# Performance work log

Measured on AMD Instinct MI355X. Metric: run time of the kernel, lower is better.

The kernel has to match this reference:

```python
import jax, jax.numpy as jnp
import numpy as np

S = 1024          # tokens (prefill)
DIM = 2560
HEAD_DIM = 128
N_HEADS = 20
N_KV = 5
HPG = N_HEADS // N_KV      # heads per kv group = 4
GS = 128                   # weight-scale group size
THETA = 500000.0
EPS = 1e-05
QKV_OUT = (N_HEADS + 2 * N_KV) * HEAD_DIM  # 3840


def setup_inputs() -> dict:
    key = jax.random.key(0)
    ks = jax.random.split(key, 7)
    x = jax.random.normal(ks[0], (S, DIM), jnp.float32)
    # unpacked int2 (ternary) weights, stored as float for the reference math
    w_qkv = jax.random.randint(ks[1], (QKV_OUT, DIM), -1, 2).astype(jnp.float32)
    ws_qkv = jax.random.uniform(ks[2], (QKV_OUT, DIM // GS), jnp.float32, 0.01, 0.05)
    w_o = jax.random.randint(ks[3], (DIM, N_HEADS * HEAD_DIM), -1, 2).astype(jnp.float32)
    ws_o = jax.random.uniform(ks[4], (DIM, N_HEADS * HEAD_DIM // GS), jnp.float32, 0.01, 0.05)
    q_norm_w = 1.0 + 0.02 * jax.random.normal(ks[5], (HEAD_DIM,), jnp.float32)
    k_norm_w = 1.0 + 0.02 * jax.random.normal(ks[6], (HEAD_DIM,), jnp.float32)
    return {"x": x, "w_qkv": w_qkv, "ws_qkv": ws_qkv, "w_o": w_o, "ws_o": ws_o,
            "q_norm_w": q_norm_w, "k_norm_w": k_norm_w}


def _quant_act(x):
    # per-token symmetric int8 quant: s = 127 / max|x| (clamped)
    s = 127.0 / jnp.clip(jnp.max(jnp.abs(x), axis=-1, keepdims=True), 1e-05, None)
    q = jnp.clip(jnp.round(x * s), -128.0, 127.0)
    return q, s


def _bitlinear(x, w, ws):
    # int8 activation x int2 weight GEMM with per-(out,group) dequant scales
    q, s = _quant_act(x)
    w_dq = w * jnp.repeat(ws, GS, axis=1)        # [out, in]
    return (q @ w_dq.T) / s


def _rmsnorm(x, w):
    return x * jax.lax.rsqrt(jnp.mean(x * x, axis=-1, keepdims=True) + EPS) * w


def _rope(x, cos, sin):
    # x: [S, ..., d]; cos/sin: [S, d//2], interleaved-pair (llama) convention
    d2 = x.shape[-1] // 2
    shape = (x.shape[0],) + (1,) * (x.ndim - 2) + (d2,)
    c = cos.reshape(shape)
    s = sin.reshape(shape)
    xr = x.reshape(x.shape[:-1] + (d2, 2))
    x0, x1 = xr[..., 0], xr[..., 1]
    out = jnp.stack([x0 * c - x1 * s, x0 * s + x1 * c], axis=-1)
    return out.reshape(x.shape)


def reference(x, w_qkv, ws_qkv, w_o, ws_o, q_norm_w, k_norm_w):
    qkv = _bitlinear(x, w_qkv, ws_qkv)                       # [S, 3840]
    q_size = N_HEADS * HEAD_DIM
    k_size = N_KV * HEAD_DIM
    xq = qkv[:, :q_size].reshape(S, N_KV, HPG, HEAD_DIM)     # [S, g, h, d]
    xk = qkv[:, q_size:q_size + k_size].reshape(S, N_KV, HEAD_DIM)
    xv = qkv[:, q_size + k_size:].reshape(S, N_KV, HEAD_DIM)
    xq = _rmsnorm(xq, q_norm_w)
    xk = _rmsnorm(xk, k_norm_w)
    # RoPE (prefill: positions 0..S-1)
    pos = jnp.arange(S, dtype=jnp.float32)
    inv_freq = THETA ** (-jnp.arange(0, HEAD_DIM, 2, dtype=jnp.float32) / HEAD_DIM)
    ang = pos[:, None] * inv_freq[None, :]                   # [S, d/2]
    cos, sin = jnp.cos(ang), jnp.sin(ang)
    xq = _rope(xq, cos, sin)
    xk = _rope(xk, cos, sin)
    # GQA causal flash-attention math
    scale = HEAD_DIM ** -0.5
    scores = jnp.einsum('sghd,tgd->ghst', xq, xk) * scale    # [g, h, S, S]
    causal = jnp.tril(jnp.ones((S, S), bool))
    scores = jnp.where(causal, scores, -1e30)
    attn = jax.nn.softmax(scores, axis=-1)
    out = jnp.einsum('ghst,tgd->sghd', attn, xv).reshape(S, N_HEADS * HEAD_DIM)
    return _bitlinear(out, w_o, ws_o)                        # [S, DIM]
```

## Files before the change

kernel.cpp:

```cpp
#include <hip/hip_runtime.h>
#include <hip/hip_bf16.h>
#include <cstdint>
#include <math.h>

#define SEQ 1024
#define DIM 2560
#define HD 128
#define NH 20
#define NKV 5
#define QKV_OUT 3840
#define GS 128

typedef __bf16 bf16;
typedef __bf16 bf16x4 __attribute__((ext_vector_type(4)));
typedef __bf16 bf16x8 __attribute__((ext_vector_type(8)));
typedef float f32x4 __attribute__((ext_vector_type(4)));

__global__ __launch_bounds__(256) void fused_pre(
    const float* __restrict__ x, bf16* __restrict__ act, float* __restrict__ rs,
    const float* __restrict__ w1, const float* __restrict__ ws1, bf16* __restrict__ o1,
    float* __restrict__ rope, long n1_4) {
  const int tid = threadIdx.x;
  if (blockIdx.x < SEQ) {
    const int row = blockIdx.x;
    const float* xr = x + (size_t)row * DIM;
    float m = 0.f;
    for (int i = tid; i < DIM; i += 256) m = fmaxf(m, fabsf(xr[i]));
    for (int off = 32; off; off >>= 1) m = fmaxf(m, __shfl_xor(m, off));
    __shared__ float red[4];
    __shared__ float s_bc;
    if ((tid & 63) == 0) red[tid >> 6] = m;
    __syncthreads();
    if (tid == 0) {
      float mm = fmaxf(fmaxf(red[0], red[1]), fmaxf(red[2], red[3]));
      mm = fmaxf(mm, 1e-5f);
      s_bc = 127.f / mm;
      rs[row] = mm / 127.f;
    }
    __syncthreads();
    const float s = s_bc;
    bf16* ar = act + (size_t)row * DIM;
    for (int i = tid; i < DIM; i += 256) {
      float q = rintf(xr[i] * s);
      q = fminf(fmaxf(q, -128.f), 127.f);
      ar[i] = (bf16)q;
    }
  } else {
    long i = (long)(blockIdx.x - SEQ) * 256 + tid;
    if (i < n1_4) {
      long e = i * 4;
      int row = (int)(e / DIM);
      int k = (int)(e % DIM);
      float sc = ws1[(size_t)row * (DIM / GS) + (k / GS)];
      float4 wv = *(const float4*)(w1 + e);
      bf16x4 ov;
      ov[0] = (bf16)(wv.x * sc);
      ov[1] = (bf16)(wv.y * sc);
      ov[2] = (bf16)(wv.z * sc);
      ov[3] = (bf16)(wv.w * sc);
      *(bf16x4*)(o1 + e) = ov;
    } else {
      long u = i - n1_4;
      if (u >= (long)SEQ * 64) return;
      int t = (int)(u >> 6), fi = (int)(u & 63);
      float inv_freq = powf(500000.f, -(float)(2 * fi) * (1.f / 128.f));
      float ang = (float)t * inv_freq;
      float sn, cs;
      sincosf(ang, &sn, &cs);
      rope[u * 2] = cs;
      rope[u * 2 + 1] = sn;
    }
  }
}

__device__ __forceinline__ void gload_lds16(const bf16* g, bf16* l) {
  __builtin_amdgcn_global_load_lds(
      (const __attribute__((address_space(1))) void*)g,
      (__attribute__((address_space(3))) void*)l, 16, 0, 0);
}

template <int BM, int BN>
__global__ __launch_bounds__(256) void gemm_pipe(
    const bf16* __restrict__ A, const bf16* __restrict__ B,
    const float* __restrict__ rs, float* __restrict__ C,
    int N, int K, int Kh, size_t part_stride, int ND, int NN) {
  constexpr int MI = BM / 32;
  constexpr int NW = BN / 32;
  constexpr int APASS = BM / 32;
  constexpr int BPASS = BN / 32;
  __shared__ bf16 As[2][BM * 64];
  __shared__ bf16 Bs[2][BN * 64];
  const int b = (int)blockIdx.x;
  const int mtile = b / ND;
  const int nz = b % ND;
  const int ntile = nz % NN;
  const int z = nz / NN;
  const int tid = threadIdx.x;
  const int w = tid >> 6, l = tid & 63;
  const int row0 = mtile * BM;
  const int col0 = ntile * BN;
  const int wm = (w >> 1) * (BM / 2), wn = (w & 1) * (BN / 2);
  const int lcol = l & 15, quad = l >> 4;
  const int sr = l >> 3, sg = l & 7;
  const bf16* Ag = A + (size_t)row0 * K + (size_t)z * Kh;
  const bf16* Bg = B + (size_t)col0 * K + (size_t)z * Kh;

  f32x4 acc[MI][NW] = {};

#define STAGE_AB(buf, k0)                                                      \
  {                                                                            \
    _Pragma("unroll") for (int i = 0; i < APASS; ++i) {                        \
      int rb = w * (BM / 4) + i * 8;                                           \
      int r = rb + sr;                                                         \
      gload_lds16(Ag + (size_t)r * K + (k0) + ((sg ^ (r & 7)) * 8),            \
                  &As[buf][rb * 64]);                                          \
    }                                                                          \
    _Pragma("unroll") for (int i = 0; i < BPASS; ++i) {                        \
      int rb = w * (BN / 4) + i * 8;                                           \
      int r = rb + sr;                                                         \
      gload_lds16(Bg + (size_t)r * K + (k0) + ((sg ^ (r & 7)) * 8),            \
                  &Bs[buf][rb * 64]);                                          \
    }                                                                          \
  }

  STAGE_AB(0, 0)
  __syncthreads();

  int buf = 0;
  for (int k0 = 0; k0 < Kh; k0 += 64) {
    if (k0 + 64 < Kh) STAGE_AB(buf ^ 1, k0 + 64)
#pragma unroll
    for (int ks = 0; ks < 2; ++ks) {
      bf16x8 af[MI], bff[NW];
#pragma unroll
      for (int mi = 0; mi < MI; ++mi) {
        int R = wm + mi * 16 + lcol;
        af[mi] = *(const bf16x8*)(&As[buf][R * 64 + (((ks * 4 + quad) ^ (R & 7)) * 8)]);
      }
#pragma unroll
      for (int ni = 0; ni < NW; ++ni) {
        int R = wn + ni * 16 + lcol;
        bff[ni] = *(const bf16x8*)(&Bs[buf][R * 64 + (((ks * 4 + quad) ^ (R & 7)) * 8)]);
      }
#pragma unroll
      for (int mi = 0; mi < MI; ++mi)
#pragma unroll
        for (int ni = 0; ni < NW; ++ni)
          acc[mi][ni] = __builtin_amdgcn_mfma_f32_16x16x32_bf16(
              af[mi], bff[ni], acc[mi][ni], 0, 0, 0);
    }
    __syncthreads();
    buf ^= 1;
  }
#undef STAGE_AB

  float* Cp = C + (size_t)z * part_stride;
#pragma unroll
  for (int mi = 0; mi < MI; ++mi) {
#pragma unroll
    for (int ni = 0; ni < NW; ++ni) {
      int col = col0 + wn + ni * 16 + lcol;
#pragma unroll
      for (int r = 0; r < 4; ++r) {
        int row = row0 + wm + mi * 16 + quad * 4 + r;
        Cp[(size_t)row * N + col] = acc[mi][ni][r] * rs[row];
      }
    }
  }
}

__global__ __launch_bounds__(256) void fused_post(
    const float* __restrict__ qkvA, const float* __restrict__ qkvB,
    const float* __restrict__ qw, const float* __restrict__ kw,
    const float* __restrict__ rope,
    bf16* __restrict__ Qo, bf16* __restrict__ Ko, bf16* __restrict__ Vt) {
  __shared__ bf16 Ls[64 * 137];
  const int bx = (int)blockIdx.x;
  const int tid = threadIdx.x;
  if (bx < 6400) {
    const int wave = tid >> 6, i = tid & 63;
    const int u = bx * 4 + wave;
    const int t = u & 1023, h = u >> 10;
    const size_t off = (h < NH)
        ? (size_t)t * QKV_OUT + h * HD
        : (size_t)t * QKV_OUT + 2560 + (h - NH) * HD;
    const float* s1 = qkvA + off;
    const float* s2 = qkvB + off;
    float2 xa = *(const float2*)(s1 + 2 * i);
    float2 xb = *(const float2*)(s2 + 2 * i);
    float x0 = xa.x + xb.x;
    float x1 = xa.y + xb.y;
    float ss = x0 * x0 + x1 * x1;
    for (int off2 = 1; off2 < 64; off2 <<= 1) ss += __shfl_xor(ss, off2);
    float r = rsqrtf(ss * (1.f / 128.f) + 1e-5f);
    const float* wv = (h < NH) ? qw : kw;
    float y0 = x0 * r * wv[2 * i];
    float y1 = x1 * r * wv[2 * i + 1];
    float2 csn = *(const float2*)(rope + ((size_t)t * 64 + i) * 2);
    float cs = csn.x, sn = csn.y;
    float o0 = y0 * cs - y1 * sn;
    float o1 = y0 * sn + y1 * cs;
    if (h < NH) {
      bf16* dst = Qo + ((size_t)t * NH + h) * HD + 2 * i;
      dst[0] = (bf16)o0; dst[1] = (bf16)o1;
    } else {
      bf16* dst = Ko + ((size_t)(h - NH) * SEQ + t) * HD + 2 * i;
      dst[0] = (bf16)o0; dst[1] = (bf16)o1;
    }
  } else {
    const int b2 = bx - 6400;
    const int t0 = (b2 & 15) * 64, g = b2 >> 4;
    {
      const int tl = tid >> 4;
      const int d0 = (tid & 15) * 8;
#pragma unroll
      for (int pass = 0; pass < 4; ++pass) {
        int t = pass * 16 + tl;
        size_t off = (size_t)(t0 + t) * QKV_OUT + 3200 + g * HD + d0;
        float4 a = *(const float4*)(qkvA + off);
        float4 b = *(const float4*)(qkvA + off + 4);
        float4 a2 = *(const float4*)(qkvB + off);
        float4 b2v = *(const float4*)(qkvB + off + 4);
        bf16* dst = Ls + t * 137 + d0;
        dst[0] = (bf16)(a.x + a2.x); dst[1] = (bf16)(a.y + a2.y);
        dst[2] = (bf16)(a.z + a2.z); dst[3] = (bf16)(a.w + a2.w);
        dst[4] = (bf16)(b.x + b2v.x); dst[5] = (bf16)(b.y + b2v.y);
        dst[6] = (bf16)(b.z + b2v.z); dst[7] = (bf16)(b.w + b2v.w);
      }
    }
    __syncthreads();
    {
      const int dl = tid >> 3;
      const int tl0 = (tid & 7) * 8;
#pragma unroll
      for (int pass = 0; pass < 4; ++pass) {
        int d = pass * 32 + dl;
        bf16x8 v;
#pragma unroll
        for (int j = 0; j < 8; ++j) v[j] = Ls[(tl0 + j) * 137 + d];
        *(bf16x8*)(Vt + ((size_t)g * HD + d) * SEQ + t0 + tl0) = v;
      }
    }
  }
}

__global__ __launch_bounds__(256, 1) void attn_mfma(
    const bf16* __restrict__ Qb, const bf16* __restrict__ Kb,
    const bf16* __restrict__ Vt, float* __restrict__ Op,
    float* __restrict__ ml,
    const float* __restrict__ w2, const float* __restrict__ ws2,
    bf16* __restrict__ o2) {
  const int bxi = (int)blockIdx.x;
  const int tid = threadIdx.x;
  if (bxi >= 600) {
    const long b2 = bxi - 600;
    const long base4 = b2 * 1024 + tid;
#pragma unroll
    for (int it = 0; it < 4; ++it) {
      long e = (base4 + it * 256) * 4;
      int row = (int)(e / DIM);
      int k = (int)(e % DIM);
      float sc = ws2[(size_t)row * (DIM / GS) + (k / GS)];
      float4 wv = *(const float4*)(w2 + e);
      bf16x4 ov;
      ov[0] = (bf16)(wv.x * sc);
      ov[1] = (bf16)(wv.y * sc);
      ov[2] = (bf16)(wv.z * sc);
      ov[3] = (bf16)(wv.w * sc);
      *(bf16x4*)(o2 + e) = ov;
    }
    return;
  }
  const int p = bxi % 60;
  const int hp = bxi / 60;
  int qb, c;
  if (p < 24)      { qb = 31 - p / 3;            c = p % 3; }
  else if (p < 48) { int r = p - 24; qb = 23 - (r >> 1); c = r & 1; }
  else             { qb = 59 - p;                c = 0; }
  const int wave = tid >> 6, lane = tid & 63;
  const int H = (hp >> 1) * 4 + (hp & 1) * 2 + (wave >> 1);
  const int g = H >> 2;
  const int qcol = lane & 15, quad = lane >> 4;
  const int q_tok = qb * 32 + (wave & 1) * 16 + qcol;
  const float scale = 0.08838834764831843f;

  __shared__ bf16 Ks[2][64 * 128];
  __shared__ bf16 Vs[2][128 * 64];

  const bf16* kbase = Kb + (size_t)g * SEQ * HD;
  const bf16* vbase = Vt + (size_t)g * HD * SEQ;

  bf16x8 qf[4];
  {
    const bf16* qp = Qb + ((size_t)q_tok * NH + H) * HD + quad * 8;
#pragma unroll
    for (int kc = 0; kc < 4; ++kc) qf[kc] = *(const bf16x8*)(qp + kc * 32);
  }

  float m_i = -1e30f, l_i = 0.f;
  f32x4 o_acc[8] = {};
  const int kt0 = c * 6;
  int kt_max = kt0 + 5;
  {
    int ktg = (qb * 32 + 31) >> 6;
    if (ktg < kt_max) kt_max = ktg;
  }

  const int k_r = lane >> 4, k_g = lane & 15;
  const int v_r = lane >> 3, v_g = lane & 7;

#define STAGE(buf, key0)                                                       \
  {                                                                            \
    _Pragma("unroll") for (int p2 = 0; p2 < 4; ++p2) {                         \
      int r0 = wave * 16 + p2 * 4;                                             \
      int r = r0 + k_r;                                                        \
      gload_lds16(kbase + (size_t)((key0) + r) * HD + ((k_g ^ (r & 15)) * 8),  \
                  &Ks[buf][r0 * 128]);                                         \
    }                                                                          \
    _Pragma("unroll") for (int p2 = 0; p2 < 4; ++p2) {                         \
      int r0 = wave * 32 + p2 * 8;                                             \
      int r = r0 + v_r;                                                        \
      gload_lds16(vbase + (size_t)r * SEQ + (key0) + ((v_g ^ (r & 7)) * 8),    \
                  &Vs[buf][r0 * 64]);                                          \
    }                                                                          \
  }

  STAGE(0, kt0 * 64)

  for (int kt = kt0; kt <= kt_max; ++kt) {
    const int key0 = kt * 64;
    __syncthreads();
    if (kt < kt_max) STAGE((kt + 1) & 1, key0 + 64)
    const bf16* Kt = Ks[kt & 1];
    const bf16* Vtile = Vs[kt & 1];

    bf16x8 kf[4][4];
#pragma unroll
    for (int mg = 0; mg < 4; ++mg) {
      const int R = mg * 16 + qcol;
      const bf16* krow = Kt + R * 128;
#pragma unroll
      for (int kc = 0; kc < 4; ++kc)
        kf[mg][kc] = *(const bf16x8*)(krow + (((kc * 4 + quad) ^ (R & 15)) * 8));
    }
    f32x4 s[4];
#pragma unroll
    for (int mg = 0; mg < 4; ++mg) {
      f32x4 acc = {0.f, 0.f, 0.f, 0.f};
#pragma unroll
      for (int kc = 0; kc < 4; ++kc)
        acc = __builtin_amdgcn_mfma_f32_16x16x32_bf16(kf[mg][kc], qf[kc], acc, 0, 0, 0);
      s[mg] = acc;
    }

    bf16x8 vf[8][2];
#pragma unroll
    for (int mg2 = 0; mg2 < 8; ++mg2) {
      const int R = mg2 * 16 + qcol;
      const bf16* vrow = Vtile + R * 64;
#pragma unroll
      for (int cc = 0; cc < 2; ++cc) {
        int g8a = cc * 8 + quad;
        int g8b = cc * 8 + 4 + quad;
        bf16x4 v0 = *(const bf16x4*)(vrow + ((g8a >> 1) ^ (R & 7)) * 8 + (g8a & 1) * 4);
        bf16x4 v1 = *(const bf16x4*)(vrow + ((g8b >> 1) ^ (R & 7)) * 8 + (g8b & 1) * 4);
#pragma unroll
        for (int j = 0; j < 4; ++j) { vf[mg2][cc][j] = v0[j]; vf[mg2][cc][j + 4] = v1[j]; }
      }
    }

    float mt = -1e30f;
#pragma unroll
    for (int mg = 0; mg < 4; ++mg)
#pragma unroll
      for (int r = 0; r < 4; ++r) {
        int key = key0 + mg * 16 + quad * 4 + r;
        float v = (key <= q_tok) ? s[mg][r] * scale : -1e30f;
        s[mg][r] = v;
        mt = fmaxf(mt, v);
      }
    mt = fmaxf(mt, __shfl_xor(mt, 16));
    mt = fmaxf(mt, __shfl_xor(mt, 32));
    float mnew = fmaxf(m_i, mt);
    float alpha = __expf(m_i - mnew);
    float ps = 0.f;
#pragma unroll
    for (int mg = 0; mg < 4; ++mg)
#pragma unroll
      for (int r = 0; r < 4; ++r) {
        float pv = __expf(s[mg][r] - mnew);
        s[mg][r] = pv;
        ps += pv;
      }
    ps += __shfl_xor(ps, 16);
    ps += __shfl_xor(ps, 32);
    l_i = l_i * alpha + ps;
    m_i = mnew;
#pragma unroll
    for (int mg2 = 0; mg2 < 8; ++mg2)
#pragma unroll
      for (int r = 0; r < 4; ++r) o_acc[mg2][r] *= alpha;

    bf16x8 pb[2];
#pragma unroll
    for (int cc = 0; cc < 2; ++cc)
#pragma unroll
      for (int j = 0; j < 8; ++j)
        pb[cc][j] = (bf16)s[cc * 2 + (j >> 2)][j & 3];

#pragma unroll
    for (int mg2 = 0; mg2 < 8; ++mg2) {
      f32x4 acc = o_acc[mg2];
#pragma unroll
      for (int cc = 0; cc < 2; ++cc)
        acc = __builtin_amdgcn_mfma_f32_16x16x32_bf16(vf[mg2][cc], pb[cc], acc, 0, 0, 0);
      o_acc[mg2] = acc;
    }
  }
#undef STAGE

  float* op = Op + ((size_t)c * SEQ + q_tok) * DIM + (size_t)H * HD + quad * 4;
#pragma unroll
  for (int mg2 = 0; mg2 < 8; ++mg2)
    *(f32x4*)(op + mg2 * 16) = o_acc[mg2];
  if (lane < 16) {
    size_t mloff = (((size_t)c * SEQ + q_tok) * NH + H) * 2;
    ml[mloff] = m_i;
    ml[mloff + 1] = l_i;
  }
}

__global__ __launch_bounds__(256) void merge_quant(
    const float* __restrict__ Op, const float* __restrict__ ml,
    bf16* __restrict__ act, float* __restrict__ rs) {
  const int t = blockIdx.x;
  const int tid = threadIdx.x;
  const int nc = (((t | 31) >> 6) / 6) + 1;
  __shared__ float sw[3][NH];
  __shared__ float red[4];
  __shared__ float s_bc;
  if (tid < NH) {
    const size_t base = ((size_t)t * NH + tid) * 2;
    const size_t cs = (size_t)SEQ * NH * 2;
    float m0 = ml[base], l0 = ml[base + 1];
    float m1 = 0.f, l1 = 0.f, m2 = 0.f, l2 = 0.f;
    float M = m0;
    if (nc > 1) { m1 = ml[base + cs];     l1 = ml[base + cs + 1];     M = fmaxf(M, m1); }
    if (nc > 2) { m2 = ml[base + 2 * cs]; l2 = ml[base + 2 * cs + 1]; M = fmaxf(M, m2); }
    float w0 = __expf(m0 - M), w1 = 0.f, w2 = 0.f;
    float L = w0 * l0;
    if (nc > 1) { w1 = __expf(m1 - M); L += w1 * l1; }
    if (nc > 2) { w2 = __expf(m2 - M); L += w2 * l2; }
    const float invL = 1.f / L;
    sw[0][tid] = w0 * invL;
    sw[1][tid] = w1 * invL;
    sw[2][tid] = w2 * invL;
  }
  __syncthreads();
  float vals[10];
  float amax = 0.f;
  const float* ob = Op + (size_t)t * DIM;
  const size_t cs = (size_t)SEQ * DIM;
#pragma unroll
  for (int j = 0; j < 10; ++j) {
    int d = j * 256 + tid;
    int h = d >> 7;
    float v = ob[d] * sw[0][h];
    if (nc > 1) v += ob[d + cs] * sw[1][h];
    if (nc > 2) v += ob[d + 2 * cs] * sw[2][h];
    vals[j] = v;
    amax = fmaxf(amax, fabsf(v));
  }
  for (int off = 32; off; off >>= 1) amax = fmaxf(amax, __shfl_xor(amax, off));
  if ((tid & 63) == 0) red[tid >> 6] = amax;
  __syncthreads();
  if (tid == 0) {
    float mm = fmaxf(fmaxf(red[0], red[1]), fmaxf(red[2], red[3]));
    mm = fmaxf(mm, 1e-5f);
    s_bc = 127.f / mm;
    rs[t] = mm / 127.f;
  }
  __syncthreads();
  const float s = s_bc;
  bf16* ar = act + (size_t)t * DIM;
#pragma unroll
  for (int j = 0; j < 10; ++j) {
    float q = rintf(vals[j] * s);
    q = fminf(fmaxf(q, -128.f), 127.f);
    ar[j * 256 + tid] = (bf16)q;
  }
}

extern "C" void kernel_launch(void* const* d_in, const int* in_sizes, int n_in,
                              void* d_out, int out_size, void* d_ws, size_t ws_size,
                              hipStream_t stream) {
  const float* x      = (const float*)d_in[0];
  const float* w_qkv  = (const float*)d_in[1];
  const float* ws_qkv = (const float*)d_in[2];
  const float* w_o    = (const float*)d_in[3];
  const float* ws_o   = (const float*)d_in[4];
  const float* qnw    = (const float*)d_in[5];
  const float* knw    = (const float*)d_in[6];
  float* out = (float*)d_out;

  char* p = (char*)d_ws;
  bf16*  act1 = (bf16*)p;  p += (size_t)SEQ * DIM * 2;
  float* rs1  = (float*)p; p += 4096;
  bf16*  wqdq = (bf16*)p;  p += (size_t)QKV_OUT * DIM * 2;
  bf16*  wodq = (bf16*)p;  p += (size_t)DIM * DIM * 2;
  float* qkvA = (float*)p; p += (size_t)SEQ * QKV_OUT * 4;
  float* qkvB = (float*)p; p += (size_t)SEQ * QKV_OUT * 4;
  bf16*  Qb   = (bf16*)p;  p += (size_t)SEQ * NH * HD * 2;
  bf16*  Kb   = (bf16*)p;  p += (size_t)NKV * SEQ * HD * 2;
  bf16*  Vt   = (bf16*)p;  p += (size_t)NKV * HD * SEQ * 2;
  bf16*  act2 = (bf16*)p;  p += (size_t)SEQ * DIM * 2;
  float* rs2  = (float*)p; p += 4096;
  float* rope = (float*)p; p += (size_t)SEQ * 64 * 2 * 4;
  float* Opart = (float*)p; p += (size_t)3 * SEQ * DIM * 4;
  float* mlbuf = (float*)p; p += (size_t)3 * SEQ * NH * 2 * 4;

  {
    long n1_4 = (long)QKV_OUT * DIM / 4;
    int dq_blocks = (int)((n1_4 + 255) / 256);
    int rope_blocks = (SEQ * 64 + 255) / 256;
    fused_pre<<<SEQ + dq_blocks + rope_blocks, 256, 0, stream>>>(
        x, act1, rs1, w_qkv, ws_qkv, wqdq, rope, n1_4);
  }
  gemm_pipe<128, 128><<<480, 256, 0, stream>>>(
      act1, wqdq, rs1, qkvA, QKV_OUT, DIM, DIM / 2, (size_t)SEQ * QKV_OUT, 60, 30);
  fused_post<<<6480, 256, 0, stream>>>(qkvA, qkvB, qnw, knw, rope, Qb, Kb, Vt);
  attn_mfma<<<2200, 256, 0, stream>>>(Qb, Kb, Vt, Opart, mlbuf, w_o, ws_o, wodq);
  merge_quant<<<SEQ, 256, 0, stream>>>(Opart, mlbuf, act2, rs2);
  gemm_pipe<64, 64><<<640, 256, 0, stream>>>(
      act2, wodq, rs2, out, DIM, DIM, DIM, 0, 40, 40);
}
```

Baseline: 217.7 us.

## Use split-K atomic GEMM with larger tiles for output projection

Replaces the 64x64 output-projection GEMM with a 128x128-tile kernel that splits K into four parts and accumulates partial results into the output with float atomics. The output buffer is zeroed by extra blocks appended to the attention launch. The aim is more data reuse per tile while keeping enough blocks to fill the GPU. The cost is atomic traffic, the extra zeroing work, and a summation order that is no longer deterministic.

```diff
diff --git a/kernel.cpp b/kernel.cpp
--- a/kernel.cpp
+++ b/kernel.cpp
@@ -164,6 +164,85 @@
       for (int r = 0; r < 4; ++r) {
         int row = row0 + wm + mi * 16 + quad * 4 + r;
         Cp[(size_t)row * N + col] = acc[mi][ni][r] * rs[row];
+      }
+    }
+  }
+}
+
+template <int BM, int BN>
+__global__ __launch_bounds__(256, 3) void gemm_atomic(
+    const bf16* __restrict__ A, const bf16* __restrict__ B,
+    const float* __restrict__ rs, float* __restrict__ C,
+    int N, int K, int Kh, int ND, int NN) {
+  constexpr int MI = BM / 32;
+  constexpr int NW = BN / 32;
+  constexpr int APASS = BM / 32;
+  constexpr int BPASS = BN / 32;
+  __shared__ bf16 As[BM * 64];
+  __shared__ bf16 Bs[BN * 64];
+  const int b = (int)blockIdx.x;
+  const int mtile = b / ND;
+  const int nz = b % ND;
+  const int ntile = nz % NN;
+  const int z = nz / NN;
+  const int tid = threadIdx.x;
+  const int w = tid >> 6, l = tid & 63;
+  const int row0 = mtile * BM;
+  const int col0 = ntile * BN;
+  const int wm = (w >> 1) * (BM / 2), wn = (w & 1) * (BN / 2);
+  const int lcol = l & 15, quad = l >> 4;
+  const int sr = l >> 3, sg = l & 7;
+  const bf16* Ag = A + (size_t)row0 * K + (size_t)z * Kh;
+  const bf16* Bg = B + (size_t)col0 * K + (size_t)z * Kh;
+
+  f32x4 acc[MI][NW] = {};
+
+  for (int k0 = 0; k0 < Kh; k0 += 64) {
+#pragma unroll
+    for (int i = 0; i < APASS; ++i) {
+      int rb = w * (BM / 4) + i * 8;
+      int r = rb + sr;
+      gload_lds16(Ag + (size_t)r * K + k0 + ((sg ^ (r & 7)) * 8), &As[rb * 64]);
+    }
+#pragma unroll
+    for (int i = 0; i < BPASS; ++i) {
+      int rb = w * (BN / 4) + i * 8;
+      int r = rb + sr;
+      gload_lds16(Bg + (size_t)r * K + k0 + ((sg ^ (r & 7)) * 8), &Bs[rb * 64]);
+    }
+    __syncthreads();
+#pragma unroll
+    for (int ks = 0; ks < 2; ++ks) {
+      bf16x8 af[MI], bff[NW];
+#pragma unroll
+      for (int mi = 0; mi < MI; ++mi) {
+        int R = wm + mi * 16 + lcol;
+        af[mi] = *(const bf16x8*)(&As[R * 64 + (((ks * 4 + quad) ^ (R & 7)) * 8)]);
+      }
+#pragma unroll
+      for (int ni = 0; ni < NW; ++ni) {
+        int R = wn + ni * 16 + lcol;
+        bff[ni] = *(const bf16x8*)(&Bs[R * 64 + (((ks * 4 + quad) ^ (R & 7)) * 8)]);
+      }
+#pragma unroll
+      for (int mi = 0; mi < MI; ++mi)
+#pragma unroll
+        for (int ni = 0; ni < NW; ++ni)
+          acc[mi][ni] = __builtin_amdgcn_mfma_f32_16x16x32_bf16(
+              af[mi], bff[ni], acc[mi][ni], 0, 0, 0);
+    }
+    __syncthreads();
+  }
+
+#pragma unroll
+  for (int mi = 0; mi < MI; ++mi) {
+#pragma unroll
+    for (int ni = 0; ni < NW; ++ni) {
+      int col = col0 + wn + ni * 16 + lcol;
+#pragma unroll
+      for (int r = 0; r < 4; ++r) {
+        int row = row0 + wm + mi * 16 + quad * 4 + r;
+        unsafeAtomicAdd(&C[(size_t)row * N + col], acc[mi][ni][r] * rs[row]);
       }
     }
   }
@@ -249,9 +328,17 @@
     const bf16* __restrict__ Vt, float* __restrict__ Op,
     float* __restrict__ ml,
     const float* __restrict__ w2, const float* __restrict__ ws2,
-    bf16* __restrict__ o2) {
+    bf16* __restrict__ o2, float* __restrict__ outz) {
   const int bxi = (int)blockIdx.x;
   const int tid = threadIdx.x;
+  if (bxi >= 2200) {
+    const long b2 = bxi - 2200;
+    f32x4 zv = {0.f, 0.f, 0.f, 0.f};
+    f32x4* dst = (f32x4*)outz + b2 * 1024 + tid;
+#pragma unroll
+    for (int it = 0; it < 4; ++it) dst[it * 256] = zv;
+    return;
+  }
   if (bxi >= 600) {
     const long b2 = bxi - 600;
     const long base4 = b2 * 1024 + tid;
@@ -529,8 +616,8 @@
   gemm_pipe<128, 128><<<480, 256, 0, stream>>>(
       act1, wqdq, rs1, qkvA, QKV_OUT, DIM, DIM / 2, (size_t)SEQ * QKV_OUT, 60, 30);
   fused_post<<<6480, 256, 0, stream>>>(qkvA, qkvB, qnw, knw, rope, Qb, Kb, Vt);
-  attn_mfma<<<2200, 256, 0, stream>>>(Qb, Kb, Vt, Opart, mlbuf, w_o, ws_o, wodq);
+  attn_mfma<<<2840, 256, 0, stream>>>(Qb, Kb, Vt, Opart, mlbuf, w_o, ws_o, wodq, out);
   merge_quant<<<SEQ, 256, 0, stream>>>(Opart, mlbuf, act2, rs2);
-  gemm_pipe<64, 64><<<640, 256, 0, stream>>>(
-      act2, wodq, rs2, out, DIM, DIM, DIM, 0, 40, 40);
-}
+  gemm_atomic<128, 128><<<640, 256, 0, stream>>>(
+      act2, wodq, rs2, out, DIM, DIM, DIM / 4, 80, 20);
+}
```

New measurement: 233.8 us. +7.4%, slower.

## Fuse QKV weight dequantization into the GEMM B-tile loads

Applied to the files above, without the earlier changes.

Removes the separate pass that dequantized the fp32 QKV weights to a bf16 workspace. The QKV GEMM now reads fp32 weights and group scales directly into registers, converts them to bf16, and writes them to LDS one stage ahead of use. This saves a full write and re-read of the dequantized weight matrix. In exchange, each of the 480 blocks (grid 8 row tiles by 60 column/K-split slots) converts fp32 weight tiles again, so every weight element is read as fp32 and converted 8 times. Register-staged loads also replace the async global-to-LDS path for B.

```diff
diff --git a/kernel.cpp b/kernel.cpp
--- a/kernel.cpp
+++ b/kernel.cpp
@@ -18,8 +18,7 @@
 
 __global__ __launch_bounds__(256) void fused_pre(
     const float* __restrict__ x, bf16* __restrict__ act, float* __restrict__ rs,
-    const float* __restrict__ w1, const float* __restrict__ ws1, bf16* __restrict__ o1,
-    float* __restrict__ rope, long n1_4) {
+    float* __restrict__ rope) {
   const int tid = threadIdx.x;
   if (blockIdx.x < SEQ) {
     const int row = blockIdx.x;
@@ -46,30 +45,15 @@
       ar[i] = (bf16)q;
     }
   } else {
-    long i = (long)(blockIdx.x - SEQ) * 256 + tid;
-    if (i < n1_4) {
-      long e = i * 4;
-      int row = (int)(e / DIM);
-      int k = (int)(e % DIM);
-      float sc = ws1[(size_t)row * (DIM / GS) + (k / GS)];
-      float4 wv = *(const float4*)(w1 + e);
-      bf16x4 ov;
-      ov[0] = (bf16)(wv.x * sc);
-      ov[1] = (bf16)(wv.y * sc);
-      ov[2] = (bf16)(wv.z * sc);
-      ov[3] = (bf16)(wv.w * sc);
-      *(bf16x4*)(o1 + e) = ov;
-    } else {
-      long u = i - n1_4;
-      if (u >= (long)SEQ * 64) return;
-      int t = (int)(u >> 6), fi = (int)(u & 63);
-      float inv_freq = powf(500000.f, -(float)(2 * fi) * (1.f / 128.f));
-      float ang = (float)t * inv_freq;
-      float sn, cs;
-      sincosf(ang, &sn, &cs);
-      rope[u * 2] = cs;
-      rope[u * 2 + 1] = sn;
-    }
+    long u = (long)(blockIdx.x - SEQ) * 256 + tid;
+    if (u >= (long)SEQ * 64) return;
+    int t = (int)(u >> 6), fi = (int)(u & 63);
+    float inv_freq = powf(500000.f, -(float)(2 * fi) * (1.f / 128.f));
+    float ang = (float)t * inv_freq;
+    float sn, cs;
+    sincosf(ang, &sn, &cs);
+    rope[u * 2] = cs;
+    rope[u * 2 + 1] = sn;
   }
 }
 
@@ -79,9 +63,10 @@
       (__attribute__((address_space(3))) void*)l, 16, 0, 0);
 }
 
-template <int BM, int BN>
+template <int BM, int BN, bool DEQB>
 __global__ __launch_bounds__(256) void gemm_pipe(
     const bf16* __restrict__ A, const bf16* __restrict__ B,
+    const float* __restrict__ Bf, const float* __restrict__ wsB,
     const float* __restrict__ rs, float* __restrict__ C,
     int N, int K, int Kh, size_t part_stride, int ND, int NN) {
   constexpr int MI = BM / 32;
@@ -107,7 +92,10 @@
 
   f32x4 acc[MI][NW] = {};
 
-#define STAGE_AB(buf, k0)                                                      \
+  float4 nb0[BPASS], nb1[BPASS];
+  float nsc[BPASS];
+
+#define STAGE_A(buf, k0)                                                       \
   {                                                                            \
     _Pragma("unroll") for (int i = 0; i < APASS; ++i) {                        \
       int rb = w * (BM / 4) + i * 8;                                           \
@@ -115,6 +103,10 @@
       gload_lds16(Ag + (size_t)r * K + (k0) + ((sg ^ (r & 7)) * 8),            \
                   &As[buf][rb * 64]);                                          \
     }                                                                          \
+  }
+
+#define STAGE_B_G(buf, k0)                                                     \
+  {                                                                            \
     _Pragma("unroll") for (int i = 0; i < BPASS; ++i) {                        \
       int rb = w * (BN / 4) + i * 8;                                           \
       int r = rb + sr;                                                         \
@@ -123,12 +115,54 @@
     }                                                                          \
   }
 
-  STAGE_AB(0, 0)
+#define LOAD_B_F32(k0)                                                         \
+  {                                                                            \
+    _Pragma("unroll") for (int i = 0; i < BPASS; ++i) {                        \
+      int rb = w * (BN / 4) + i * 8;                                           \
+      int r = rb + sr;                                                         \
+      int kk = (k0) + ((sg ^ (r & 7)) * 8);                                    \
+      const float* src = Bf + (size_t)(col0 + r) * K + (size_t)z * Kh + kk;    \
+      nb0[i] = *(const float4*)src;                                            \
+      nb1[i] = *(const float4*)(src + 4);                                      \
+      nsc[i] = wsB[(size_t)(col0 + r) * (K / GS) + ((z * Kh + (k0)) >> 7)];    \
+    }                                                                          \
+  }
+
+#define WRITE_B_LDS(buf)                                                       \
+  {                                                                            \
+    _Pragma("unroll") for (int i = 0; i < BPASS; ++i) {                        \
+      int rb = w * (BN / 4) + i * 8;                                           \
+      int r = rb + sr;                                                         \
+      float sc = nsc[i];                                                       \
+      bf16x8 dv;                                                               \
+      dv[0] = (bf16)(nb0[i].x * sc); dv[1] = (bf16)(nb0[i].y * sc);            \
+      dv[2] = (bf16)(nb0[i].z * sc); dv[3] = (bf16)(nb0[i].w * sc);            \
+      dv[4] = (bf16)(nb1[i].x * sc); dv[5] = (bf16)(nb1[i].y * sc);            \
+      dv[6] = (bf16)(nb1[i].z * sc); dv[7] = (bf16)(nb1[i].w * sc);            \
+      *(bf16x8*)(&Bs[buf][r * 64 + sg * 8]) = dv;                              \
+    }                                                                          \
+  }
+
+  STAGE_A(0, 0)
+  if constexpr (DEQB) {
+    LOAD_B_F32(0)
+    WRITE_B_LDS(0)
+  } else {
+    STAGE_B_G(0, 0)
+  }
   __syncthreads();
 
   int buf = 0;
   for (int k0 = 0; k0 < Kh; k0 += 64) {
-    if (k0 + 64 < Kh) STAGE_AB(buf ^ 1, k0 + 64)
+    const bool pref = (k0 + 64 < Kh);
+    if (pref) {
+      STAGE_A(buf ^ 1, k0 + 64)
+      if constexpr (DEQB) {
+        LOAD_B_F32(k0 + 64)
+      } else {
+        STAGE_B_G(buf ^ 1, k0 + 64)
+      }
+    }
 #pragma unroll
     for (int ks = 0; ks < 2; ++ks) {
       bf16x8 af[MI], bff[NW];
@@ -149,10 +183,16 @@
           acc[mi][ni] = __builtin_amdgcn_mfma_f32_16x16x32_bf16(
               af[mi], bff[ni], acc[mi][ni], 0, 0, 0);
     }
+    if (pref) {
+      if constexpr (DEQB) WRITE_B_LDS(buf ^ 1)
+    }
     __syncthreads();
     buf ^= 1;
   }
-#undef STAGE_AB
+#undef STAGE_A
+#undef STAGE_B_G
+#undef LOAD_B_F32
+#undef WRITE_B_LDS
 
   float* Cp = C + (size_t)z * part_stride;
 #pragma unroll
@@ -506,7 +546,6 @@
   char* p = (char*)d_ws;
   bf16*  act1 = (bf16*)p;  p += (size_t)SEQ * DIM * 2;
   float* rs1  = (float*)p; p += 4096;
-  bf16*  wqdq = (bf16*)p;  p += (size_t)QKV_OUT * DIM * 2;
   bf16*  wodq = (bf16*)p;  p += (size_t)DIM * DIM * 2;
   float* qkvA = (float*)p; p += (size_t)SEQ * QKV_OUT * 4;
   float* qkvB = (float*)p; p += (size_t)SEQ * QKV_OUT * 4;
@@ -519,18 +558,13 @@
   float* Opart = (float*)p; p += (size_t)3 * SEQ * DIM * 4;
   float* mlbuf = (float*)p; p += (size_t)3 * SEQ * NH * 2 * 4;
 
-  {
-    long n1_4 = (long)QKV_OUT * DIM / 4;
-    int dq_blocks = (int)((n1_4 + 255) / 256);
-    int rope_blocks = (SEQ * 64 + 255) / 256;
-    fused_pre<<<SEQ + dq_blocks + rope_blocks, 256, 0, stream>>>(
-        x, act1, rs1, w_qkv, ws_qkv, wqdq, rope, n1_4);
-  }
-  gemm_pipe<128, 128><<<480, 256, 0, stream>>>(
-      act1, wqdq, rs1, qkvA, QKV_OUT, DIM, DIM / 2, (size_t)SEQ * QKV_OUT, 60, 30);
+  fused_pre<<<SEQ + 256, 256, 0, stream>>>(x, act1, rs1, rope);
+  gemm_pipe<128, 128, true><<<480, 256, 0, stream>>>(
+      act1, nullptr, w_qkv, ws_qkv, rs1, qkvA, QKV_OUT, DIM, DIM / 2,
+      (size_t)SEQ * QKV_OUT, 60, 30);
   fused_post<<<6480, 256, 0, stream>>>(qkvA, qkvB, qnw, knw, rope, Qb, Kb, Vt);
   attn_mfma<<<2200, 256, 0, stream>>>(Qb, Kb, Vt, Opart, mlbuf, w_o, ws_o, wodq);
   merge_quant<<<SEQ, 256, 0, stream>>>(Opart, mlbuf, act2, rs2);
-  gemm_pipe<64, 64><<<640, 256, 0, stream>>>(
-      act2, wodq, rs2, out, DIM, DIM, DIM, 0, 40, 40);
-}
+  gemm_pipe<64, 64, false><<<640, 256, 0, stream>>>(
+      act2, wodq, nullptr, nullptr, rs2, out, DIM, DIM, DIM, 0, 40, 40);
+}
```

After: 230.6 us. 1.06x slower.

## Fuse QKV GEMM epilogue with RMSNorm, RoPE and V transpose, drop split-K

Applied to the files above, without the earlier changes.

Replaces the split-K QKV GEMM and separate post-processing kernel with one GEMM using 64x128 tiles, where each N tile is exactly one head. The epilogue computes the per-head RMSNorm through shuffles and shared memory, applies RoPE, and writes bf16 Q/K or transposed V directly. This removes the two fp32 partial buffers, their round-trip through memory, and one kernel launch. In exchange each block now runs the full K loop, so blocks are longer with no split-K parallelism.

```diff
diff --git a/kernel.cpp b/kernel.cpp
--- a/kernel.cpp
+++ b/kernel.cpp
@@ -79,11 +79,190 @@
       (__attribute__((address_space(3))) void*)l, 16, 0, 0);
 }
 
+__global__ __launch_bounds__(256) void gemm1_fused(
+    const bf16* __restrict__ A, const bf16* __restrict__ B,
+    const float* __restrict__ rs, const float* __restrict__ qw,
+    const float* __restrict__ kw, const float* __restrict__ rope,
+    bf16* __restrict__ Qo, bf16* __restrict__ Ko, bf16* __restrict__ Vt) {
+  constexpr int BM = 64, BN = 128, MI = 2, NW = 4;
+  __shared__ bf16 As[2][BM * 64];
+  __shared__ bf16 Bs[2][BN * 64];
+  __shared__ float ssred[BM][2];
+  const int b = (int)blockIdx.x;
+  const int mtile = b / 30, ntile = b % 30;
+  const int tid = threadIdx.x;
+  const int w = tid >> 6, l = tid & 63;
+  const int row0 = mtile * BM;
+  const int col0 = ntile * BN;
+  const int wm = (w >> 1) * 32, wn = (w & 1) * 64;
+  const int lcol = l & 15, quad = l >> 4;
+  const int sr = l >> 3, sg = l & 7;
+  const bf16* Ag = A + (size_t)row0 * DIM;
+  const bf16* Bg = B + (size_t)col0 * DIM;
+
+  f32x4 acc[MI][NW] = {};
+
+#define STAGE1(buf, k0)                                                        \
+  {                                                                            \
+    _Pragma("unroll") for (int i = 0; i < 2; ++i) {                            \
+      int rb = w * 16 + i * 8;                                                 \
+      int r = rb + sr;                                                         \
+      gload_lds16(Ag + (size_t)r * DIM + (k0) + ((sg ^ (r & 7)) * 8),          \
+                  &As[buf][rb * 64]);                                          \
+    }                                                                          \
+    _Pragma("unroll") for (int i = 0; i < 4; ++i) {                            \
+      int rb = w * 32 + i * 8;                                                 \
+      int r = rb + sr;                                                         \
+      gload_lds16(Bg + (size_t)r * DIM + (k0) + ((sg ^ (r & 7)) * 8),          \
+                  &Bs[buf][rb * 64]);                                          \
+    }                                                                          \
+  }
+
+  STAGE1(0, 0)
+  __syncthreads();
+
+  int buf = 0;
+  for (int k0 = 0; k0 < DIM; k0 += 64) {
+    if (k0 + 64 < DIM) STAGE1(buf ^ 1, k0 + 64)
+#pragma unroll
+    for (int ks = 0; ks < 2; ++ks) {
+      bf16x8 af[MI], bff[NW];
+#pragma unroll
+      for (int mi = 0; mi < MI; ++mi) {
+        int R = wm + mi * 16 + lcol;
+        af[mi] = *(const bf16x8*)(&As[buf][R * 64 + (((ks * 4 + quad) ^ (R & 7)) * 8)]);
+      }
+#pragma unroll
+      for (int ni = 0; ni < NW; ++ni) {
+        int R = wn + ni * 16 + lcol;
+        bff[ni] = *(const bf16x8*)(&Bs[buf][R * 64 + (((ks * 4 + quad) ^ (R & 7)) * 8)]);
+      }
+#pragma unroll
+      for (int mi = 0; mi < MI; ++mi)
+#pragma unroll
+        for (int ni = 0; ni < NW; ++ni)
+          acc[mi][ni] = __builtin_amdgcn_mfma_f32_16x16x32_bf16(
+              af[mi], bff[ni], acc[mi][ni], 0, 0, 0);
+    }
+    __syncthreads();
+    buf ^= 1;
+  }
+#undef STAGE1
+
+  float rsr[MI][4];
+#pragma unroll
+  for (int mi = 0; mi < MI; ++mi)
+#pragma unroll
+    for (int r = 0; r < 4; ++r)
+      rsr[mi][r] = rs[row0 + wm + mi * 16 + quad * 4 + r];
+#pragma unroll
+  for (int mi = 0; mi < MI; ++mi)
+#pragma unroll
+    for (int ni = 0; ni < NW; ++ni)
+#pragma unroll
+      for (int r = 0; r < 4; ++r)
+        acc[mi][ni][r] *= rsr[mi][r];
+
+  const bool isV = (ntile >= 25);
+  const bool isK = (ntile >= 20) && !isV;
+
+  if (!isV) {
+#pragma unroll
+    for (int mi = 0; mi < MI; ++mi)
+#pragma unroll
+      for (int r = 0; r < 4; ++r) {
+        float s = 0.f;
+#pragma unroll
+        for (int ni = 0; ni < NW; ++ni) {
+          float v = acc[mi][ni][r];
+          s += v * v;
+        }
+        s += __shfl_xor(s, 1);
+        s += __shfl_xor(s, 2);
+        s += __shfl_xor(s, 4);
+        s += __shfl_xor(s, 8);
+        if (lcol == 0) ssred[wm + mi * 16 + quad * 4 + r][w & 1] = s;
+      }
+  }
+  __syncthreads();
+
+  bf16* Ls = &Bs[0][0];
+  if (!isV) {
+    float rms[MI][4];
+#pragma unroll
+    for (int mi = 0; mi < MI; ++mi)
+#pragma unroll
+      for (int r = 0; r < 4; ++r) {
+        int row = wm + mi * 16 + quad * 4 + r;
+        float t = ssred[row][0] + ssred[row][1];
+        rms[mi][r] = rsqrtf(t * (1.f / 128.f) + 1e-5f);
+      }
+    const float* nw = isK ? kw : qw;
+    float nwv[NW];
+#pragma unroll
+    for (int ni = 0; ni < NW; ++ni) nwv[ni] = nw[wn + ni * 16 + lcol];
+#pragma unroll
+    for (int mi = 0; mi < MI; ++mi)
+#pragma unroll
+      for (int ni = 0; ni < NW; ++ni)
+#pragma unroll
+        for (int r = 0; r < 4; ++r) {
+          int row = wm + mi * 16 + quad * 4 + r;
+          int d = wn + ni * 16 + lcol;
+          float y = acc[mi][ni][r] * rms[mi][r] * nwv[ni];
+          float2 csn = *(const float2*)(
+              rope + (((size_t)(row0 + row)) * 64 + (d >> 1)) * 2);
+          float pv = __shfl_xor(y, 1);
+          y = (lcol & 1) ? (pv * csn.y + y * csn.x)
+                         : (y * csn.x - pv * csn.y);
+          Ls[row * 137 + d] = (bf16)y;
+        }
+  } else {
+#pragma unroll
+    for (int mi = 0; mi < MI; ++mi)
+#pragma unroll
+      for (int ni = 0; ni < NW; ++ni)
+#pragma unroll
+        for (int r = 0; r < 4; ++r) {
+          int row = wm + mi * 16 + quad * 4 + r;
+          int d = wn + ni * 16 + lcol;
+          Ls[row * 137 + d] = (bf16)acc[mi][ni][r];
+        }
+  }
+  __syncthreads();
+
+  if (!isV) {
+#pragma unroll
+    for (int pass = 0; pass < 4; ++pass) {
+      int row = pass * 16 + (tid >> 4);
+      int d0 = (tid & 15) * 8;
+      bf16x8 v;
+#pragma unroll
+      for (int j = 0; j < 8; ++j) v[j] = Ls[row * 137 + d0 + j];
+      int t = row0 + row;
+      bf16* dst = isK ? (Ko + ((size_t)(ntile - 20) * SEQ + t) * HD + d0)
+                      : (Qo + ((size_t)t * NH + ntile) * HD + d0);
+      *(bf16x8*)dst = v;
+    }
+  } else {
+    const int g = ntile - 25;
+#pragma unroll
+    for (int pass = 0; pass < 4; ++pass) {
+      int d = pass * 32 + (tid >> 3);
+      int tl0 = (tid & 7) * 8;
+      bf16x8 v;
+#pragma unroll
+      for (int j = 0; j < 8; ++j) v[j] = Ls[(tl0 + j) * 137 + d];
+      *(bf16x8*)(Vt + ((size_t)g * HD + d) * SEQ + row0 + tl0) = v;
+    }
+  }
+}
+
 template <int BM, int BN>
 __global__ __launch_bounds__(256) void gemm_pipe(
     const bf16* __restrict__ A, const bf16* __restrict__ B,
     const float* __restrict__ rs, float* __restrict__ C,
-    int N, int K, int Kh, size_t part_stride, int ND, int NN) {
+    int N, int K, int ND, int NN) {
   constexpr int MI = BM / 32;
   constexpr int NW = BN / 32;
   constexpr int APASS = BM / 32;
@@ -92,9 +271,7 @@
   __shared__ bf16 Bs[2][BN * 64];
   const int b = (int)blockIdx.x;
   const int mtile = b / ND;
-  const int nz = b % ND;
-  const int ntile = nz % NN;
-  const int z = nz / NN;
+  const int ntile = b % ND % NN;
   const int tid = threadIdx.x;
   const int w = tid >> 6, l = tid & 63;
   const int row0 = mtile * BM;
@@ -102,8 +279,8 @@
   const int wm = (w >> 1) * (BM / 2), wn = (w & 1) * (BN / 2);
   const int lcol = l & 15, quad = l >> 4;
   const int sr = l >> 3, sg = l & 7;
-  const bf16* Ag = A + (size_t)row0 * K + (size_t)z * Kh;
-  const bf16* Bg = B + (size_t)col0 * K + (size_t)z * Kh;
+  const bf16* Ag = A + (size_t)row0 * K;
+  const bf16* Bg = B + (size_t)col0 * K;
 
   f32x4 acc[MI][NW] = {};
 
@@ -127,8 +304,8 @@
   __syncthreads();
 
   int buf = 0;
-  for (int k0 = 0; k0 < Kh; k0 += 64) {
-    if (k0 + 64 < Kh) STAGE_AB(buf ^ 1, k0 + 64)
+  for (int k0 = 0; k0 < K; k0 += 64) {
+    if (k0 + 64 < K) STAGE_AB(buf ^ 1, k0 + 64)
 #pragma unroll
     for (int ks = 0; ks < 2; ++ks) {
       bf16x8 af[MI], bff[NW];
@@ -154,7 +331,6 @@
   }
 #undef STAGE_AB
 
-  float* Cp = C + (size_t)z * part_stride;
 #pragma unroll
   for (int mi = 0; mi < MI; ++mi) {
 #pragma unroll
@@ -163,82 +339,7 @@
 #pragma unroll
       for (int r = 0; r < 4; ++r) {
         int row = row0 + wm + mi * 16 + quad * 4 + r;
-        Cp[(size_t)row * N + col] = acc[mi][ni][r] * rs[row];
-      }
-    }
-  }
-}
-
-__global__ __launch_bounds__(256) void fused_post(
-    const float* __restrict__ qkvA, const float* __restrict__ qkvB,
-    const float* __restrict__ qw, const float* __restrict__ kw,
-    const float* __restrict__ rope,
-    bf16* __restrict__ Qo, bf16* __restrict__ Ko, bf16* __restrict__ Vt) {
-  __shared__ bf16 Ls[64 * 137];
-  const int bx = (int)blockIdx.x;
-  const int tid = threadIdx.x;
-  if (bx < 6400) {
-    const int wave = tid >> 6, i = tid & 63;
-    const int u = bx * 4 + wave;
-    const int t = u & 1023, h = u >> 10;
-    const size_t off = (h < NH)
-        ? (size_t)t * QKV_OUT + h * HD
-        : (size_t)t * QKV_OUT + 2560 + (h - NH) * HD;
-    const float* s1 = qkvA + off;
-    const float* s2 = qkvB + off;
-    float2 xa = *(const float2*)(s1 + 2 * i);
-    float2 xb = *(const float2*)(s2 + 2 * i);
-    float x0 = xa.x + xb.x;
-    float x1 = xa.y + xb.y;
-    float ss = x0 * x0 + x1 * x1;
-    for (int off2 = 1; off2 < 64; off2 <<= 1) ss += __shfl_xor(ss, off2);
-    float r = rsqrtf(ss * (1.f / 128.f) + 1e-5f);
-    const float* wv = (h < NH) ? qw : kw;
-    float y0 = x0 * r * wv[2 * i];
-    float y1 = x1 * r * wv[2 * i + 1];
-    float2 csn = *(const float2*)(rope + ((size_t)t * 64 + i) * 2);
-    float cs = csn.x, sn = csn.y;
-    float o0 = y0 * cs - y1 * sn;
-    float o1 = y0 * sn + y1 * cs;
-    if (h < NH) {
-      bf16* dst = Qo + ((size_t)t * NH + h) * HD + 2 * i;
-      dst[0] = (bf16)o0; dst[1] = (bf16)o1;
-    } else {
-      bf16* dst = Ko + ((size_t)(h - NH) * SEQ + t) * HD + 2 * i;
-      dst[0] = (bf16)o0; dst[1] = (bf16)o1;
-    }
-  } else {
-    const int b2 = bx - 6400;
-    const int t0 = (b2 & 15) * 64, g = b2 >> 4;
-    {
-      const int tl = tid >> 4;
-      const int d0 = (tid & 15) * 8;
-#pragma unroll
-      for (int pass = 0; pass < 4; ++pass) {
-        int t = pass * 16 + tl;
-        size_t off = (size_t)(t0 + t) * QKV_OUT + 3200 + g * HD + d0;
-        float4 a = *(const float4*)(qkvA + off);
-        float4 b = *(const float4*)(qkvA + off + 4);
-        float4 a2 = *(const float4*)(qkvB + off);
-        float4 b2v = *(const float4*)(qkvB + off + 4);
-        bf16* dst = Ls + t * 137 + d0;
-        dst[0] = (bf16)(a.x + a2.x); dst[1] = (bf16)(a.y + a2.y);
-        dst[2] = (bf16)(a.z + a2.z); dst[3] = (bf16)(a.w + a2.w);
-        dst[4] = (bf16)(b.x + b2v.x); dst[5] = (bf16)(b.y + b2v.y);
-        dst[6] = (bf16)(b.z + b2v.z); dst[7] = (bf16)(b.w + b2v.w);
-      }
-    }
-    __syncthreads();
-    {
-      const int dl = tid >> 3;
-      const int tl0 = (tid & 7) * 8;
-#pragma unroll
-      for (int pass = 0; pass < 4; ++pass) {
-        int d = pass * 32 + dl;
-        bf16x8 v;
-#pragma unroll
-        for (int j = 0; j < 8; ++j) v[j] = Ls[(tl0 + j) * 137 + d];
-        *(bf16x8*)(Vt + ((size_t)g * HD + d) * SEQ + t0 + tl0) = v;
+        C[(size_t)row * N + col] = acc[mi][ni][r] * rs[row];
       }
     }
   }
@@ -508,8 +609,6 @@
   float* rs1  = (float*)p; p += 4096;
   bf16*  wqdq = (bf16*)p;  p += (size_t)QKV_OUT * DIM * 2;
   bf16*  wodq = (bf16*)p;  p += (size_t)DIM * DIM * 2;
-  float* qkvA = (float*)p; p += (size_t)SEQ * QKV_OUT * 4;
-  float* qkvB = (float*)p; p += (size_t)SEQ * QKV_OUT * 4;
   bf16*  Qb   = (bf16*)p;  p += (size_t)SEQ * NH * HD * 2;
   bf16*  Kb   = (bf16*)p;  p += (size_t)NKV * SEQ * HD * 2;
   bf16*  Vt   = (bf16*)p;  p += (size_t)NKV * HD * SEQ * 2;
@@ -526,11 +625,10 @@
     fused_pre<<<SEQ + dq_blocks + rope_blocks, 256, 0, stream>>>(
         x, act1, rs1, w_qkv, ws_qkv, wqdq, rope, n1_4);
   }
-  gemm_pipe<128, 128><<<480, 256, 0, stream>>>(
-      act1, wqdq, rs1, qkvA, QKV_OUT, DIM, DIM / 2, (size_t)SEQ * QKV_OUT, 60, 30);
-  fused_post<<<6480, 256, 0, stream>>>(qkvA, qkvB, qnw, knw, rope, Qb, Kb, Vt);
+  gemm1_fused<<<480, 256, 0, stream>>>(
+      act1, wqdq, rs1, qnw, knw, rope, Qb, Kb, Vt);
   attn_mfma<<<2200, 256, 0, stream>>>(Qb, Kb, Vt, Opart, mlbuf, w_o, ws_o, wodq);
   merge_quant<<<SEQ, 256, 0, stream>>>(Opart, mlbuf, act2, rs2);
   gemm_pipe<64, 64><<<640, 256, 0, stream>>>(
-      act2, wodq, rs2, out, DIM, DIM, DIM, 0, 40, 40);
+      act2, wodq, rs2, out, DIM, DIM, 40, 40);
 }
```

Result: slower. 223.1 us (+2.5%).
